# Kernel optimization log

Hardware: AMD Instinct MI355X
Metric: run time of the kernel (lower is better)

Reference implementation:

```python
import jax, jax.numpy as jnp
import numpy as np

DIM = 768
NUM_HEADS = 8
HEAD_DIM = DIM // NUM_HEADS


def setup_inputs() -> dict:
    key = jax.random.key(0)
    k1, k2, k3, k4, k5 = jax.random.split(key, 5)
    B, C, H, W = 16, DIM, 32, 32
    x = jax.random.normal(k1, (B, C, H, W), dtype=jnp.float32)
    # Conv2d 1x1 weights expressed as [out_ch, in_ch] matrices
    w_qkv = jax.random.normal(k2, (3 * C, C), dtype=jnp.float32) * (C ** -0.5)
    b_qkv = jax.random.normal(k3, (3 * C,), dtype=jnp.float32) * 0.02
    w_proj = jax.random.normal(k4, (C, C), dtype=jnp.float32) * (C ** -0.5)
    b_proj = jax.random.normal(k5, (C,), dtype=jnp.float32) * 0.02
    return {"x": x, "w_qkv": w_qkv, "b_qkv": b_qkv, "w_proj": w_proj, "b_proj": b_proj}


def reference(x, w_qkv, b_qkv, w_proj, b_proj):
    B, C, H, W = x.shape
    N = H * W
    nh, hd = NUM_HEADS, C // NUM_HEADS
    xf = x.astype(jnp.float32).reshape(B, C, N)  # bcn
    # 1x1 conv == channel matmul
    qkv = jnp.einsum('oc,bcn->bon', w_qkv, xf) + b_qkv[None, :, None]
    qkv = qkv.reshape(B, 3, nh, hd, N)
    q, k, v = qkv[:, 0], qkv[:, 1], qkv[:, 2]  # [B, nh, hd, N]
    s = hd ** -0.25  # scale split between q and k as in the original
    attn = jnp.einsum('bhdn,bhdm->bhnm', q * s, k * s)  # [B, nh, N, N]
    attn = attn - jax.lax.stop_gradient(jnp.max(attn, axis=-1, keepdims=True))
    attn = jnp.clip(attn, -88.0, 88.0)
    attn = jax.nn.softmax(attn, axis=-1)
    # dropout is identity in eval mode
    out = jnp.einsum('bhnm,bhdm->bhdn', attn, v)  # [B, nh, hd, N]
    out = out.reshape(B, C, N)
    out = jnp.einsum('oc,bcn->bon', w_proj, out) + b_proj[None, :, None]
    return out.reshape(B, C, H, W).astype(x.dtype)
```

## Files before the change

### kernel.cpp

```cpp
#include <hip/hip_runtime.h>
#include <stdint.h>

typedef __attribute__((ext_vector_type(4))) float f32x4;
typedef __attribute__((ext_vector_type(16))) float f32x16;
typedef __attribute__((ext_vector_type(8))) short bf16x8;

#define SQKV 0.38372606f
#define RM 8.0f

__device__ __forceinline__ unsigned short f2bf(float f) {
  union { float f; unsigned u; } v; v.f = f;
  unsigned r = v.u + 0x7FFFu + ((v.u >> 16) & 1u);
  return (unsigned short)(r >> 16);
}

__device__ __forceinline__ unsigned cvt_pk_bf16(float a, float b) {
  unsigned r;
  asm volatile("v_cvt_pk_bf16_f32 %0, %1, %2" : "=v"(r) : "v"(a), "v"(b));
  return r;
}
__device__ __forceinline__ void permswap(unsigned &a, unsigned &b) {
  asm volatile("v_permlane32_swap_b32 %0, %1" : "+v"(a), "+v"(b));
}

__device__ __forceinline__ void glds16(const unsigned short* g, unsigned short* l) {
  __builtin_amdgcn_global_load_lds(
      (const __attribute__((address_space(1))) void*)g,
      (__attribute__((address_space(3))) void*)l, 16, 0, 0);
}

__global__ __launch_bounds__(256) void k_convert2(const float* __restrict__ s1,
                                                  const float* __restrict__ s2,
                                                  unsigned short* __restrict__ d1,
                                                  int n1_4, int ntot4) {
  int i = blockIdx.x * 256 + threadIdx.x;
  if (i >= ntot4) return;
  const float4 v = (i < n1_4) ? reinterpret_cast<const float4*>(s1)[i]
                              : reinterpret_cast<const float4*>(s2)[i - n1_4];
  ushort4 o;
  o.x = f2bf(v.x); o.y = f2bf(v.y); o.z = f2bf(v.z); o.w = f2bf(v.w);
  reinterpret_cast<ushort4*>(d1)[i] = o;
}

__global__ __launch_bounds__(256) void k_transpose(const float* __restrict__ x,
                                                   unsigned short* __restrict__ xT) {
  __shared__ float tile[32][33];
  const int t = threadIdx.x;
  const int n0 = blockIdx.x * 32, c0 = blockIdx.y * 32, b = blockIdx.z;
  const int lc = t >> 3, ln = (t & 7) * 4;
  const float4 v = *reinterpret_cast<const float4*>(
      x + ((size_t)b * 768 + c0 + lc) * 1024 + n0 + ln);
  tile[lc][ln] = v.x; tile[lc][ln + 1] = v.y;
  tile[lc][ln + 2] = v.z; tile[lc][ln + 3] = v.w;
  __syncthreads();
  const int sn = t >> 3, sc = (t & 7) * 4;
  ushort4 o;
  o.x = f2bf(tile[sc][sn]);     o.y = f2bf(tile[sc + 1][sn]);
  o.z = f2bf(tile[sc + 2][sn]); o.w = f2bf(tile[sc + 3][sn]);
  *reinterpret_cast<ushort4*>(xT + ((size_t)b * 1024 + n0 + sn) * 768 + c0 + sc) = o;
}

__global__ __launch_bounds__(256, 2) void k_gemm_qkv(
    const unsigned short* __restrict__ A,
    const unsigned short* __restrict__ Bx,
    const float* __restrict__ bias,
    unsigned short* __restrict__ qT,
    unsigned short* __restrict__ kT,
    unsigned short* __restrict__ vO) {
  __shared__ unsigned short As[3 * 8192];
  __shared__ unsigned short Bs[3 * 4096];
  const int t = threadIdx.x;
  const int tm = blockIdx.x >> 7;
  const int tn = blockIdx.x & 127;
  const int lane = t & 63, w = t >> 6;
  const int wm = w >> 1, wn = w & 1;
  const int w512 = w * 512;

  const int sr = t >> 2;
  const int sg8 = ((t & 3) ^ ((t >> 3) & 3)) << 3;
  const unsigned short* aLo = A + (size_t)(tm * 256 + sr) * 768 + sg8;
  const unsigned short* bLo = Bx + ((size_t)tn * 128 + sr) * 768 + sg8;

  f32x4 acc[8][4];
#pragma unroll
  for (int mi = 0; mi < 8; ++mi)
#pragma unroll
    for (int ni = 0; ni < 4; ++ni) acc[mi][ni] = (f32x4)0.0f;

  const int rp = ((lane >> 4) ^ ((lane >> 1) & 3)) << 3;
  const int arowoff = (wm * 128 + (lane & 15)) * 32 + rp;
  const int browoff = (wn * 64 + (lane & 15)) * 32 + rp;

  auto stage = [&](int j, int bf) {
    const size_t ko = (size_t)j * 32;
    glds16(aLo + ko,               As + bf * 8192 + w512);
    glds16(aLo + ko +  64 * 768,   As + bf * 8192 + 2048 + w512);
    glds16(aLo + ko + 128 * 768,   As + bf * 8192 + 4096 + w512);
    glds16(aLo + ko + 192 * 768,   As + bf * 8192 + 6144 + w512);
    glds16(bLo + ko,               Bs + bf * 4096 + w512);
    glds16(bLo + ko +  64 * 768,   Bs + bf * 4096 + 2048 + w512);
  };

  stage(0, 0); stage(1, 1); stage(2, 2);

  int buf = 0;
  for (int kt = 0; kt < 24; ++kt) {
    if (kt < 22)      asm volatile("s_waitcnt vmcnt(12)" ::: "memory");
    else if (kt == 22) asm volatile("s_waitcnt vmcnt(6)" ::: "memory");
    else               asm volatile("s_waitcnt vmcnt(0)" ::: "memory");
    asm volatile("s_barrier" ::: "memory");

    const unsigned short* Ab = As + buf * 8192 + arowoff;
    const unsigned short* Bb = Bs + buf * 4096 + browoff;
    bf16x8 bfr[4], af[4];
#pragma unroll
    for (int ni = 0; ni < 4; ++ni)
      bfr[ni] = *reinterpret_cast<const bf16x8*>(Bb + ni * 512);
#pragma unroll
    for (int mi = 0; mi < 4; ++mi)
      af[mi] = *reinterpret_cast<const bf16x8*>(Ab + mi * 512);
    __builtin_amdgcn_s_setprio(1);
#pragma unroll
    for (int mi = 0; mi < 4; ++mi)
#pragma unroll
      for (int ni = 0; ni < 4; ++ni)
        acc[mi][ni] = __builtin_amdgcn_mfma_f32_16x16x32_bf16(af[mi], bfr[ni], acc[mi][ni], 0, 0, 0);
    __builtin_amdgcn_s_setprio(0);
#pragma unroll
    for (int mi = 0; mi < 4; ++mi)
      af[mi] = *reinterpret_cast<const bf16x8*>(Ab + (mi + 4) * 512);
    __builtin_amdgcn_s_setprio(1);
#pragma unroll
    for (int mi = 0; mi < 4; ++mi)
#pragma unroll
      for (int ni = 0; ni < 4; ++ni)
        acc[mi + 4][ni] = __builtin_amdgcn_mfma_f32_16x16x32_bf16(af[mi], bfr[ni], acc[mi + 4][ni], 0, 0, 0);
    __builtin_amdgcn_s_setprio(0);

    asm volatile("s_waitcnt lgkmcnt(0)" ::: "memory");
    asm volatile("s_barrier" ::: "memory");
    if (kt < 21) stage(kt + 3, buf);
    buf = (buf == 2) ? 0 : buf + 1;
  }

  const int b = tn >> 3;
#pragma unroll
  for (int mi = 0; mi < 8; ++mi) {
    const int o0 = tm * 256 + wm * 128 + mi * 16 + ((lane >> 4) << 2);
    const float4 bb = *reinterpret_cast<const float4*>(bias + o0);
    const float sc = (o0 < 1536) ? SQKV : 1.0f;
    const int om = o0 % 768;
    const int hh = om / 96;
    const int d0 = om % 96;
    const int region = o0 / 768;
    const size_t bh = (size_t)(b * 8 + hh);
#pragma unroll
    for (int ni = 0; ni < 4; ++ni) {
      const int nn = (tn & 7) * 128 + wn * 64 + ni * 16 + (lane & 15);
      ushort4 st;
      st.x = f2bf((acc[mi][ni][0] + bb.x) * sc);
      st.y = f2bf((acc[mi][ni][1] + bb.y) * sc);
      st.z = f2bf((acc[mi][ni][2] + bb.z) * sc);
      st.w = f2bf((acc[mi][ni][3] + bb.w) * sc);
      if (region == 0) {
        *reinterpret_cast<ushort4*>(qT + (bh * 1024 + nn) * 96 + d0) = st;
      } else if (region == 1) {
        *reinterpret_cast<ushort4*>(kT + (bh * 1024 + nn) * 96 + d0) = st;
      } else {
        unsigned short* vp = vO + (bh * 96 + d0) * 1024 + nn;
        vp[0] = st.x; vp[1024] = st.y; vp[2048] = st.z; vp[3072] = st.w;
      }
    }
  }
}

__global__ __launch_bounds__(256, 2) void k_attn3(
    const unsigned short* __restrict__ qT,
    const unsigned short* __restrict__ kT,
    const unsigned short* __restrict__ vO,
    unsigned short* __restrict__ attoutT) {
  __shared__ unsigned short Ks[2][64 * 104];
  __shared__ unsigned short Vs[2][96 * 72];
  __shared__ float redbuf[4][2][32];

  const int t = threadIdx.x, lane = t & 63, wv = t >> 6;
  const int r31 = lane & 31, h = lane >> 5;
  const int sw = (blockIdx.x & 7) * 64 + (blockIdx.x >> 3);
  const int bh = sw >> 2, qt = sw & 3;
  const int b = bh >> 3, hh = bh & 7;
  const int n0 = qt * 256 + wv * 64;

  bf16x8 Qf0[6], Qf1[6];
  {
    const unsigned short* q0 = qT + ((size_t)bh * 1024 + n0 + r31) * 96 + h * 8;
    const unsigned short* q1 = q0 + (size_t)32 * 96;
#pragma unroll
    for (int ks = 0; ks < 6; ++ks) {
      Qf0[ks] = *reinterpret_cast<const bf16x8*>(q0 + ks * 16);
      Qf1[ks] = *reinterpret_cast<const bf16x8*>(q1 + ks * 16);
    }
  }

  const unsigned short* gptr[6];
  unsigned short* lptr[6];
#pragma unroll
  for (int i = 0; i < 6; ++i) {
    if (i < 3) {
      const int cc = t + i * 256;
      const int row = cc / 12, col = (cc % 12) * 8;
      gptr[i] = kT + ((size_t)bh * 1024 + row) * 96 + col;
      lptr[i] = &Ks[0][row * 104 + col];
    } else {
      const int cv = t + (i - 3) * 256;
      const int d = cv >> 3, col = (cv & 7) * 8;
      gptr[i] = vO + ((size_t)bh * 96 + d) * 1024 + col;
      lptr[i] = &Vs[0][d * 72 + col];
    }
  }
  uint4 rg[6];
#pragma unroll
  for (int i = 0; i < 6; ++i) rg[i] = *reinterpret_cast<const uint4*>(gptr[i]);

  f32x16 oac0[3], oac1[3];
#pragma unroll
  for (int dt = 0; dt < 3; ++dt) { oac0[dt] = (f32x16)0.0f; oac1[dt] = (f32x16)0.0f; }
  float run_l0 = 0.0f, run_l1 = 0.0f;

  int cur = 0;
  for (int it = 0; it < 16; ++it, cur ^= 1) {
#pragma unroll
    for (int i = 0; i < 6; ++i)
      *reinterpret_cast<uint4*>(lptr[i] + cur * (i < 3 ? 64 * 104 : 96 * 72)) = rg[i];
    __syncthreads();
    if (it < 15) {
#pragma unroll
      for (int i = 0; i < 6; ++i) {
        gptr[i] += (i < 3) ? 64 * 96 : 64;
        rg[i] = *reinterpret_cast<const uint4*>(gptr[i]);
      }
    }
    const unsigned short* Kb = &Ks[cur][0];
    const unsigned short* Vb = &Vs[cur][0];

    union { bf16x8 v; unsigned u[4]; } pf0, pf1;

    {
      f32x16 sa0 = (f32x16)0.0f, sa1 = (f32x16)0.0f;
      __builtin_amdgcn_s_setprio(1);
#pragma unroll
      for (int ks = 0; ks < 6; ++ks) {
        const bf16x8 k0 = *reinterpret_cast<const bf16x8*>(Kb + r31 * 104 + ks * 16 + h * 8);
        sa0 = __builtin_amdgcn_mfma_f32_32x32x16_bf16(k0, Qf0[ks], sa0, 0, 0, 0);
        sa1 = __builtin_amdgcn_mfma_f32_32x32x16_bf16(k0, Qf1[ks], sa1, 0, 0, 0);
      }
      __builtin_amdgcn_s_setprio(0);

      float t0 = 0.f, t1 = 0.f, u0 = 0.f, u1 = 0.f;
#pragma unroll
      for (int i = 0; i < 16; i += 2) {
        sa0[i]     = __builtin_amdgcn_exp2f(sa0[i] - RM);     t0 += sa0[i];
        sa0[i + 1] = __builtin_amdgcn_exp2f(sa0[i + 1] - RM); t1 += sa0[i + 1];
        sa1[i]     = __builtin_amdgcn_exp2f(sa1[i] - RM);     u0 += sa1[i];
        sa1[i + 1] = __builtin_amdgcn_exp2f(sa1[i + 1] - RM); u1 += sa1[i + 1];
      }
      float ts = t0 + t1, us = u0 + u1;
      ts += __shfl_xor(ts, 32);
      us += __shfl_xor(us, 32);
      run_l0 += ts; run_l1 += us;

#pragma unroll
      for (int kst = 0; kst < 2; ++kst) {
        const int base = kst * 8;
        {
          unsigned X = cvt_pk_bf16(sa0[base + 0], sa0[base + 1]);
          unsigned Y = cvt_pk_bf16(sa0[base + 2], sa0[base + 3]);
          unsigned Z = cvt_pk_bf16(sa0[base + 4], sa0[base + 5]);
          unsigned W = cvt_pk_bf16(sa0[base + 6], sa0[base + 7]);
          permswap(X, Z); permswap(Y, W);
          pf0.u[0] = X; pf0.u[1] = Y; pf0.u[2] = Z; pf0.u[3] = W;
        }
        {
          unsigned X = cvt_pk_bf16(sa1[base + 0], sa1[base + 1]);
          unsigned Y = cvt_pk_bf16(sa1[base + 2], sa1[base + 3]);
          unsigned Z = cvt_pk_bf16(sa1[base + 4], sa1[base + 5]);
          unsigned W = cvt_pk_bf16(sa1[base + 6], sa1[base + 7]);
          permswap(X, Z); permswap(Y, W);
          pf1.u[0] = X; pf1.u[1] = Y; pf1.u[2] = Z; pf1.u[3] = W;
        }
#pragma unroll
        for (int dt = 0; dt < 3; ++dt) {
          const bf16x8 vf = *reinterpret_cast<const bf16x8*>(
              Vb + (dt * 32 + r31) * 72 + kst * 16 + h * 8);
          oac0[dt] = __builtin_amdgcn_mfma_f32_32x32x16_bf16(pf0.v, vf, oac0[dt], 0, 0, 0);
          oac1[dt] = __builtin_amdgcn_mfma_f32_32x32x16_bf16(pf1.v, vf, oac1[dt], 0, 0, 0);
        }
      }
    }

    {
      f32x16 sb0 = (f32x16)0.0f, sb1 = (f32x16)0.0f;
      __builtin_amdgcn_s_setprio(1);
#pragma unroll
      for (int ks = 0; ks < 6; ++ks) {
        const bf16x8 k1 = *reinterpret_cast<const bf16x8*>(Kb + (32 + r31) * 104 + ks * 16 + h * 8);
        sb0 = __builtin_amdgcn_mfma_f32_32x32x16_bf16(k1, Qf0[ks], sb0, 0, 0, 0);
        sb1 = __builtin_amdgcn_mfma_f32_32x32x16_bf16(k1, Qf1[ks], sb1, 0, 0, 0);
      }
      __builtin_amdgcn_s_setprio(0);

      float t0 = 0.f, t1 = 0.f, u0 = 0.f, u1 = 0.f;
#pragma unroll
      for (int i = 0; i < 16; i += 2) {
        sb0[i]     = __builtin_amdgcn_exp2f(sb0[i] - RM);     t0 += sb0[i];
        sb0[i + 1] = __builtin_amdgcn_exp2f(sb0[i + 1] - RM); t1 += sb0[i + 1];
        sb1[i]     = __builtin_amdgcn_exp2f(sb1[i] - RM);     u0 += sb1[i];
        sb1[i + 1] = __builtin_amdgcn_exp2f(sb1[i + 1] - RM); u1 += sb1[i + 1];
      }
      float ts = t0 + t1, us = u0 + u1;
      ts += __shfl_xor(ts, 32);
      us += __shfl_xor(us, 32);
      run_l0 += ts; run_l1 += us;

#pragma unroll
      for (int kst = 2; kst < 4; ++kst) {
        const int base = (kst & 1) * 8;
        {
          unsigned X = cvt_pk_bf16(sb0[base + 0], sb0[base + 1]);
          unsigned Y = cvt_pk_bf16(sb0[base + 2], sb0[base + 3]);
          unsigned Z = cvt_pk_bf16(sb0[base + 4], sb0[base + 5]);
          unsigned W = cvt_pk_bf16(sb0[base + 6], sb0[base + 7]);
          permswap(X, Z); permswap(Y, W);
          pf0.u[0] = X; pf0.u[1] = Y; pf0.u[2] = Z; pf0.u[3] = W;
        }
        {
          unsigned X = cvt_pk_bf16(sb1[base + 0], sb1[base + 1]);
          unsigned Y = cvt_pk_bf16(sb1[base + 2], sb1[base + 3]);
          unsigned Z = cvt_pk_bf16(sb1[base + 4], sb1[base + 5]);
          unsigned W = cvt_pk_bf16(sb1[base + 6], sb1[base + 7]);
          permswap(X, Z); permswap(Y, W);
          pf1.u[0] = X; pf1.u[1] = Y; pf1.u[2] = Z; pf1.u[3] = W;
        }
#pragma unroll
        for (int dt = 0; dt < 3; ++dt) {
          const bf16x8 vf = *reinterpret_cast<const bf16x8*>(
              Vb + (dt * 32 + r31) * 72 + kst * 16 + h * 8);
          oac0[dt] = __builtin_amdgcn_mfma_f32_32x32x16_bf16(pf0.v, vf, oac0[dt], 0, 0, 0);
          oac1[dt] = __builtin_amdgcn_mfma_f32_32x32x16_bf16(pf1.v, vf, oac1[dt], 0, 0, 0);
        }
      }
    }
  }

  if (lane < 32) redbuf[wv][0][lane] = 1.0f / run_l0;
  else           redbuf[wv][1][r31]  = 1.0f / run_l1;
  f32x4 i40[4], i41[4];
#pragma unroll
  for (int q = 0; q < 4; ++q) {
    i40[q] = *reinterpret_cast<const f32x4*>(&redbuf[wv][0][q * 8 + h * 4]);
    i41[q] = *reinterpret_cast<const f32x4*>(&redbuf[wv][1][q * 8 + h * 4]);
  }
  unsigned short* ob0 = attoutT + ((size_t)b * 1024 + n0) * 768 + hh * 96;
  unsigned short* ob1 = ob0 + (size_t)32 * 768;
#pragma unroll
  for (int dt = 0; dt < 3; ++dt)
#pragma unroll
    for (int q = 0; q < 4; ++q)
#pragma unroll
      for (int j = 0; j < 4; ++j) {
        const int np = q * 8 + h * 4 + j;
        ob0[(size_t)np * 768 + dt * 32 + r31] = f2bf(oac0[dt][q * 4 + j] * i40[q][j]);
        ob1[(size_t)np * 768 + dt * 32 + r31] = f2bf(oac1[dt][q * 4 + j] * i41[q][j]);
      }
}

__global__ __launch_bounds__(256, 4) void k_gemm_proj(
    const unsigned short* __restrict__ Aat,
    const unsigned short* __restrict__ Bw,
    const float* __restrict__ bias,
    float* __restrict__ out) {
  __shared__ unsigned short As[2 * 128 * 32];
  __shared__ unsigned short Bs[2 * 128 * 32];
  const int t = threadIdx.x;
  const int b = blockIdx.y;
  const int tm = blockIdx.x / 6, tn = blockIdx.x % 6;
  const int lane = t & 63, w = t >> 6, wr = w >> 1, wc = w & 1;

  const int srow = 16 * w + (lane >> 2);
  const int sg = (lane & 3) ^ ((lane >> 3) & 3);
  const int scol = sg << 3;
  const unsigned short* aptr0 = Aat + (size_t)b * 1024 * 768 + (size_t)(tm * 128 + srow) * 768 + scol;
  const unsigned short* aptr1 = aptr0 + (size_t)64 * 768;
  const unsigned short* bptr0 = Bw + (size_t)(tn * 128 + srow) * 768 + scol;
  const unsigned short* bptr1 = bptr0 + (size_t)64 * 768;
  unsigned short* const lA0 = As + 512 * w;
  unsigned short* const lA1 = As + 2048 + 512 * w;
  unsigned short* const lB0 = Bs + 512 * w;
  unsigned short* const lB1 = Bs + 2048 + 512 * w;

  f32x4 acc[4][4];
#pragma unroll
  for (int mi = 0; mi < 4; ++mi)
#pragma unroll
    for (int ni = 0; ni < 4; ++ni) acc[mi][ni] = (f32x4)0.0f;

  const int rp = ((lane >> 4) ^ ((lane >> 1) & 3)) << 3;
  const unsigned short* rA[4];
  const unsigned short* rB[4];
#pragma unroll
  for (int mi = 0; mi < 4; ++mi)
    rA[mi] = As + (wr * 64 + mi * 16 + (lane & 15)) * 32 + rp;
#pragma unroll
  for (int ni = 0; ni < 4; ++ni)
    rB[ni] = Bs + (wc * 64 + ni * 16 + (lane & 15)) * 32 + rp;

  glds16(aptr0, lA0);
  glds16(aptr1, lA1);
  glds16(bptr0, lB0);
  glds16(bptr1, lB1);
  aptr0 += 32; aptr1 += 32; bptr0 += 32; bptr1 += 32;

  for (int kt = 0; kt < 24; ++kt) {
    const int cur = kt & 1, nxt = (kt & 1) ^ 1;
    __syncthreads();
    if (kt < 23) {
      glds16(aptr0, lA0 + nxt * 4096);
      glds16(aptr1, lA1 + nxt * 4096);
      glds16(bptr0, lB0 + nxt * 4096);
      glds16(bptr1, lB1 + nxt * 4096);
      aptr0 += 32; aptr1 += 32; bptr0 += 32; bptr1 += 32;
    }

    bf16x8 af[4], bfr[4];
#pragma unroll
    for (int mi = 0; mi < 4; ++mi)
      af[mi] = *reinterpret_cast<const bf16x8*>(rA[mi] + cur * 4096);
#pragma unroll
    for (int ni = 0; ni < 4; ++ni)
      bfr[ni] = *reinterpret_cast<const bf16x8*>(rB[ni] + cur * 4096);
#pragma unroll
    for (int mi = 0; mi < 4; ++mi)
#pragma unroll
      for (int ni = 0; ni < 4; ++ni)
        acc[mi][ni] = __builtin_amdgcn_mfma_f32_16x16x32_bf16(af[mi], bfr[ni], acc[mi][ni], 0, 0, 0);
  }

#pragma unroll
  for (int mi = 0; mi < 4; ++mi) {
    const int n0 = tm * 128 + wr * 64 + mi * 16 + ((lane >> 4) << 2);
#pragma unroll
    for (int ni = 0; ni < 4; ++ni) {
      const int o = tn * 128 + wc * 64 + ni * 16 + (lane & 15);
      const float bo = bias[o];
      float4 vv;
      vv.x = acc[mi][ni][0] + bo;
      vv.y = acc[mi][ni][1] + bo;
      vv.z = acc[mi][ni][2] + bo;
      vv.w = acc[mi][ni][3] + bo;
      *reinterpret_cast<float4*>(out + ((size_t)b * 768 + o) * 1024 + n0) = vv;
    }
  }
}

extern "C" void kernel_launch(void* const* d_in, const int* in_sizes, int n_in,
                              void* d_out, int out_size, void* d_ws, size_t ws_size,
                              hipStream_t stream) {
  const float* x = (const float*)d_in[0];
  const float* w_qkv = (const float*)d_in[1];
  const float* b_qkv = (const float*)d_in[2];
  const float* w_proj = (const float*)d_in[3];
  const float* b_proj = (const float*)d_in[4];
  float* out = (float*)d_out;

  unsigned short* ws = (unsigned short*)d_ws;
  unsigned short* wqkv_bf = ws;
  unsigned short* wproj_bf = wqkv_bf + 2304 * 768;
  unsigned short* xT = wproj_bf + 768 * 768;
  unsigned short* qT = xT + (size_t)16 * 1024 * 768;
  unsigned short* kT = qT + (size_t)16 * 8 * 1024 * 96;
  unsigned short* vO = kT + (size_t)16 * 8 * 1024 * 96;
  unsigned short* attoutT = xT;

  const int n1_4 = 2304 * 768 / 4;
  const int ntot4 = n1_4 + 768 * 768 / 4;
  k_convert2<<<(ntot4 + 255) / 256, 256, 0, stream>>>(w_qkv, w_proj, wqkv_bf, n1_4, ntot4);
  k_transpose<<<dim3(32, 24, 16), 256, 0, stream>>>(x, xT);
  k_gemm_qkv<<<1152, 256, 0, stream>>>(wqkv_bf, xT, b_qkv, qT, kT, vO);
  k_attn3<<<512, 256, 0, stream>>>(qT, kT, vO, attoutT);
  k_gemm_proj<<<dim3(48, 16), 256, 0, stream>>>(attoutT, wproj_bf, b_proj, out);
}
```

Measured before the change: 215.7 us.

## Merge prep kernels and retile QKV GEMM to 256x256 tiles with 512 threads

Fuses the weight conversion and x transpose into one prep launch, removing one kernel launch. Rewrites the QKV GEMM to use 256x256 output tiles with 8 waves, BK=64 double buffering, and a phased schedule that issues the next loads in the middle of MFMA work. Larger tiles cut global traffic per FLOP. The cost is more LDS per block (128KB) and fewer blocks in flight, which may limit occupancy, and the new pipelining is more involved.

Result: slower. 226.6 us (+5.0%).

```diff
diff --git a/kernel.cpp b/kernel.cpp
--- a/kernel.cpp
+++ b/kernel.cpp
@@ -29,57 +29,114 @@
       (__attribute__((address_space(3))) void*)l, 16, 0, 0);
 }
 
-__global__ __launch_bounds__(256) void k_convert2(const float* __restrict__ s1,
-                                                  const float* __restrict__ s2,
-                                                  unsigned short* __restrict__ d1,
-                                                  int n1_4, int ntot4) {
-  int i = blockIdx.x * 256 + threadIdx.x;
-  if (i >= ntot4) return;
-  const float4 v = (i < n1_4) ? reinterpret_cast<const float4*>(s1)[i]
-                              : reinterpret_cast<const float4*>(s2)[i - n1_4];
-  ushort4 o;
-  o.x = f2bf(v.x); o.y = f2bf(v.y); o.z = f2bf(v.z); o.w = f2bf(v.w);
-  reinterpret_cast<ushort4*>(d1)[i] = o;
-}
-
-__global__ __launch_bounds__(256) void k_transpose(const float* __restrict__ x,
-                                                   unsigned short* __restrict__ xT) {
+__global__ __launch_bounds__(256) void k_prep(const float* __restrict__ x,
+                                              const float* __restrict__ w_qkv,
+                                              const float* __restrict__ w_proj,
+                                              unsigned short* __restrict__ xT,
+                                              unsigned short* __restrict__ wbf,
+                                              int n1_4, int ntot4) {
   __shared__ float tile[32][33];
+  const int bid = blockIdx.x;
   const int t = threadIdx.x;
-  const int n0 = blockIdx.x * 32, c0 = blockIdx.y * 32, b = blockIdx.z;
-  const int lc = t >> 3, ln = (t & 7) * 4;
-  const float4 v = *reinterpret_cast<const float4*>(
-      x + ((size_t)b * 768 + c0 + lc) * 1024 + n0 + ln);
-  tile[lc][ln] = v.x; tile[lc][ln + 1] = v.y;
-  tile[lc][ln + 2] = v.z; tile[lc][ln + 3] = v.w;
-  __syncthreads();
-  const int sn = t >> 3, sc = (t & 7) * 4;
-  ushort4 o;
-  o.x = f2bf(tile[sc][sn]);     o.y = f2bf(tile[sc + 1][sn]);
-  o.z = f2bf(tile[sc + 2][sn]); o.w = f2bf(tile[sc + 3][sn]);
-  *reinterpret_cast<ushort4*>(xT + ((size_t)b * 1024 + n0 + sn) * 768 + c0 + sc) = o;
-}
-
-__global__ __launch_bounds__(256, 2) void k_gemm_qkv(
+  if (bid < 12288) {
+    const int bx = bid & 31, rest = bid >> 5;
+    const int by = rest % 24, bz = rest / 24;
+    const int n0 = bx * 32, c0 = by * 32, b = bz;
+    const int lc = t >> 3, ln = (t & 7) * 4;
+    const float4 v = *reinterpret_cast<const float4*>(
+        x + ((size_t)b * 768 + c0 + lc) * 1024 + n0 + ln);
+    tile[lc][ln] = v.x; tile[lc][ln + 1] = v.y;
+    tile[lc][ln + 2] = v.z; tile[lc][ln + 3] = v.w;
+    __syncthreads();
+    const int sn = t >> 3, sc = (t & 7) * 4;
+    ushort4 o;
+    o.x = f2bf(tile[sc][sn]);     o.y = f2bf(tile[sc + 1][sn]);
+    o.z = f2bf(tile[sc + 2][sn]); o.w = f2bf(tile[sc + 3][sn]);
+    *reinterpret_cast<ushort4*>(xT + ((size_t)b * 1024 + n0 + sn) * 768 + c0 + sc) = o;
+  } else {
+    const int i = (bid - 12288) * 256 + t;
+    if (i < ntot4) {
+      const float4 v = (i < n1_4) ? reinterpret_cast<const float4*>(w_qkv)[i]
+                                  : reinterpret_cast<const float4*>(w_proj)[i - n1_4];
+      ushort4 o;
+      o.x = f2bf(v.x); o.y = f2bf(v.y); o.z = f2bf(v.z); o.w = f2bf(v.w);
+      reinterpret_cast<ushort4*>(wbf)[i] = o;
+    }
+  }
+}
+
+#define STG(SLOT, HALF, KTG)                                                        \
+  { const size_t ko = (size_t)(KTG) * 64;                                           \
+    glds16(Abase + (size_t)((HALF) * 128) * 768 + ko,                               \
+           SMw + (SLOT) * 16384 + (HALF) * 8192);                                   \
+    glds16(Abase + (size_t)((HALF) * 128 + 64) * 768 + ko,                          \
+           SMw + (SLOT) * 16384 + (HALF) * 8192 + 4096);                            \
+    glds16(Bbase + (size_t)((HALF) * 128) * 768 + ko,                               \
+           SMw + 32768 + (SLOT) * 16384 + (HALF) * 8192);                           \
+    glds16(Bbase + (size_t)((HALF) * 128 + 64) * 768 + ko,                          \
+           SMw + 32768 + (SLOT) * 16384 + (HALF) * 8192 + 4096); }
+
+#define QPHASE(S, MH, NH, STAGE_CODE, DRAIN_CODE)                                   \
+  {                                                                                 \
+    const unsigned short* aB = SM + (S) * 16384 + (wm * 128 + (MH) * 64 + lq) * 64; \
+    const unsigned short* bB = SM + 32768 + (S) * 16384 + (wc * 64 + (NH) * 32 + lq) * 64; \
+    bf16x8 af[4][2], bv[2][2];                                                      \
+    _Pragma("unroll")                                                               \
+    for (int mi = 0; mi < 4; ++mi) {                                                \
+      af[mi][0] = *(const bf16x8*)(aB + mi * 1024 + physK0);                        \
+      af[mi][1] = *(const bf16x8*)(aB + mi * 1024 + physK1);                        \
+    }                                                                               \
+    _Pragma("unroll")                                                               \
+    for (int ni = 0; ni < 2; ++ni) {                                                \
+      bv[ni][0] = *(const bf16x8*)(bB + ni * 1024 + physK0);                        \
+      bv[ni][1] = *(const bf16x8*)(bB + ni * 1024 + physK1);                        \
+    }                                                                               \
+    STAGE_CODE;                                                                     \
+    asm volatile("s_barrier" ::: "memory");                                         \
+    asm volatile("s_waitcnt lgkmcnt(0)" ::: "memory");                              \
+    __builtin_amdgcn_sched_barrier(0);                                              \
+    __builtin_amdgcn_s_setprio(1);                                                  \
+    _Pragma("unroll")                                                               \
+    for (int mi = 0; mi < 4; ++mi)                                                  \
+      _Pragma("unroll")                                                             \
+      for (int ni = 0; ni < 2; ++ni) {                                              \
+        acc[(MH) * 4 + mi][(NH) * 2 + ni] = __builtin_amdgcn_mfma_f32_16x16x32_bf16(\
+            af[mi][0], bv[ni][0], acc[(MH) * 4 + mi][(NH) * 2 + ni], 0, 0, 0);      \
+        acc[(MH) * 4 + mi][(NH) * 2 + ni] = __builtin_amdgcn_mfma_f32_16x16x32_bf16(\
+            af[mi][1], bv[ni][1], acc[(MH) * 4 + mi][(NH) * 2 + ni], 0, 0, 0);      \
+      }                                                                             \
+    __builtin_amdgcn_s_setprio(0);                                                  \
+    __builtin_amdgcn_sched_barrier(0);                                              \
+    DRAIN_CODE;                                                                     \
+    asm volatile("s_barrier" ::: "memory");                                         \
+  }
+
+#define QNOP ((void)0)
+#define QDRAIN asm volatile("s_waitcnt vmcnt(0)" ::: "memory")
+
+__global__ __launch_bounds__(512, 2) void k_gemm_qkv(
     const unsigned short* __restrict__ A,
     const unsigned short* __restrict__ Bx,
     const float* __restrict__ bias,
     unsigned short* __restrict__ qT,
     unsigned short* __restrict__ kT,
     unsigned short* __restrict__ vO) {
-  __shared__ unsigned short As[3 * 8192];
-  __shared__ unsigned short Bs[3 * 4096];
+  __shared__ unsigned short SM[65536];
   const int t = threadIdx.x;
-  const int tm = blockIdx.x >> 7;
-  const int tn = blockIdx.x & 127;
+  const int tm = blockIdx.x >> 6;
+  const int tn = blockIdx.x & 63;
   const int lane = t & 63, w = t >> 6;
-  const int wm = w >> 1, wn = w & 1;
-  const int w512 = w * 512;
-
-  const int sr = t >> 2;
-  const int sg8 = ((t & 3) ^ ((t >> 3) & 3)) << 3;
-  const unsigned short* aLo = A + (size_t)(tm * 256 + sr) * 768 + sg8;
-  const unsigned short* bLo = Bx + ((size_t)tn * 128 + sr) * 768 + sg8;
+  const int wm = w >> 2, wc = w & 3;
+  const int lq = lane & 15;
+
+  const int srow = w * 8 + (lane >> 3);
+  const int sgsrc = ((lane & 7) ^ ((lane >> 3) & 7)) << 3;
+  const unsigned short* Abase = A + (size_t)(tm * 256 + srow) * 768 + sgsrc;
+  const unsigned short* Bbase = Bx + (size_t)(tn * 256 + srow) * 768 + sgsrc;
+  unsigned short* const SMw = SM + w * 512;
+
+  const int physK0 = (((lane >> 4)) ^ (lane & 7)) << 3;
+  const int physK1 = ((4 + (lane >> 4)) ^ (lane & 7)) << 3;
 
   f32x4 acc[8][4];
 #pragma unroll
@@ -87,63 +144,25 @@
 #pragma unroll
     for (int ni = 0; ni < 4; ++ni) acc[mi][ni] = (f32x4)0.0f;
 
-  const int rp = ((lane >> 4) ^ ((lane >> 1) & 3)) << 3;
-  const int arowoff = (wm * 128 + (lane & 15)) * 32 + rp;
-  const int browoff = (wn * 64 + (lane & 15)) * 32 + rp;
-
-  auto stage = [&](int j, int bf) {
-    const size_t ko = (size_t)j * 32;
-    glds16(aLo + ko,               As + bf * 8192 + w512);
-    glds16(aLo + ko +  64 * 768,   As + bf * 8192 + 2048 + w512);
-    glds16(aLo + ko + 128 * 768,   As + bf * 8192 + 4096 + w512);
-    glds16(aLo + ko + 192 * 768,   As + bf * 8192 + 6144 + w512);
-    glds16(bLo + ko,               Bs + bf * 4096 + w512);
-    glds16(bLo + ko +  64 * 768,   Bs + bf * 4096 + 2048 + w512);
-  };
-
-  stage(0, 0); stage(1, 1); stage(2, 2);
-
-  int buf = 0;
-  for (int kt = 0; kt < 24; ++kt) {
-    if (kt < 22)      asm volatile("s_waitcnt vmcnt(12)" ::: "memory");
-    else if (kt == 22) asm volatile("s_waitcnt vmcnt(6)" ::: "memory");
-    else               asm volatile("s_waitcnt vmcnt(0)" ::: "memory");
-    asm volatile("s_barrier" ::: "memory");
-
-    const unsigned short* Ab = As + buf * 8192 + arowoff;
-    const unsigned short* Bb = Bs + buf * 4096 + browoff;
-    bf16x8 bfr[4], af[4];
-#pragma unroll
-    for (int ni = 0; ni < 4; ++ni)
-      bfr[ni] = *reinterpret_cast<const bf16x8*>(Bb + ni * 512);
-#pragma unroll
-    for (int mi = 0; mi < 4; ++mi)
-      af[mi] = *reinterpret_cast<const bf16x8*>(Ab + mi * 512);
-    __builtin_amdgcn_s_setprio(1);
-#pragma unroll
-    for (int mi = 0; mi < 4; ++mi)
-#pragma unroll
-      for (int ni = 0; ni < 4; ++ni)
-        acc[mi][ni] = __builtin_amdgcn_mfma_f32_16x16x32_bf16(af[mi], bfr[ni], acc[mi][ni], 0, 0, 0);
-    __builtin_amdgcn_s_setprio(0);
-#pragma unroll
-    for (int mi = 0; mi < 4; ++mi)
-      af[mi] = *reinterpret_cast<const bf16x8*>(Ab + (mi + 4) * 512);
-    __builtin_amdgcn_s_setprio(1);
-#pragma unroll
-    for (int mi = 0; mi < 4; ++mi)
-#pragma unroll
-      for (int ni = 0; ni < 4; ++ni)
-        acc[mi + 4][ni] = __builtin_amdgcn_mfma_f32_16x16x32_bf16(af[mi], bfr[ni], acc[mi + 4][ni], 0, 0, 0);
-    __builtin_amdgcn_s_setprio(0);
-
-    asm volatile("s_waitcnt lgkmcnt(0)" ::: "memory");
-    asm volatile("s_barrier" ::: "memory");
-    if (kt < 21) stage(kt + 3, buf);
-    buf = (buf == 2) ? 0 : buf + 1;
-  }
-
-  const int b = tn >> 3;
+  STG(0, 0, 0);
+  STG(0, 1, 0);
+  asm volatile("s_waitcnt vmcnt(0)" ::: "memory");
+  asm volatile("s_barrier" ::: "memory");
+
+#pragma unroll 1
+  for (int it = 0; it < 6; ++it) {
+    const int kg1 = 2 * it + 1, kg2 = 2 * it + 2;
+    QPHASE(0, 0, 0, STG(1, 0, kg1), QNOP);
+    QPHASE(0, 0, 1, STG(1, 1, kg1), QNOP);
+    QPHASE(0, 1, 0, QNOP, QNOP);
+    QPHASE(0, 1, 1, QNOP, QDRAIN);
+    QPHASE(1, 0, 0, if (it < 5) STG(0, 0, kg2), QNOP);
+    QPHASE(1, 0, 1, if (it < 5) STG(0, 1, kg2), QNOP);
+    QPHASE(1, 1, 0, QNOP, QNOP);
+    QPHASE(1, 1, 1, QNOP, QDRAIN);
+  }
+
+  const int b = tn >> 2;
 #pragma unroll
   for (int mi = 0; mi < 8; ++mi) {
     const int o0 = tm * 256 + wm * 128 + mi * 16 + ((lane >> 4) << 2);
@@ -156,7 +175,7 @@
     const size_t bh = (size_t)(b * 8 + hh);
 #pragma unroll
     for (int ni = 0; ni < 4; ++ni) {
-      const int nn = (tn & 7) * 128 + wn * 64 + ni * 16 + (lane & 15);
+      const int nn = (tn & 3) * 256 + wc * 64 + ni * 16 + (lane & 15);
       ushort4 st;
       st.x = f2bf((acc[mi][ni][0] + bb.x) * sc);
       st.y = f2bf((acc[mi][ni][1] + bb.y) * sc);
@@ -482,9 +501,9 @@
 
   const int n1_4 = 2304 * 768 / 4;
   const int ntot4 = n1_4 + 768 * 768 / 4;
-  k_convert2<<<(ntot4 + 255) / 256, 256, 0, stream>>>(w_qkv, w_proj, wqkv_bf, n1_4, ntot4);
-  k_transpose<<<dim3(32, 24, 16), 256, 0, stream>>>(x, xT);
-  k_gemm_qkv<<<1152, 256, 0, stream>>>(wqkv_bf, xT, b_qkv, qT, kT, vO);
+  const int nconv_blocks = (ntot4 + 255) / 256;
+  k_prep<<<12288 + nconv_blocks, 256, 0, stream>>>(x, w_qkv, w_proj, xT, wqkv_bf, n1_4, ntot4);
+  k_gemm_qkv<<<576, 512, 0, stream>>>(wqkv_bf, xT, b_qkv, qT, kT, vO);
   k_attn3<<<512, 256, 0, stream>>>(qT, kT, vO, attoutT);
   k_gemm_proj<<<dim3(48, 16), 256, 0, stream>>>(attoutT, wproj_bf, b_proj, out);
 }
```
